# Performance work log

Hardware: AMD Instinct MI355X
Metric: run time of the kernel (lower is better)

Reference implementation:

```python
import jax, jax.numpy as jnp
import numpy as np

DIM = 1024
H = 16
HD = DIM // H
SCALE = HD ** -0.5
LAMBDA_INIT = 0.1
EPS = 1e-6


def setup_inputs() -> dict:
    key0 = jax.random.key(0)
    ks = jax.random.split(key0, 12)
    B, Nq, Nk = 2, 1024, 2048
    w = 0.02
    inp = {
        "query": jax.random.normal(ks[0], (B, Nq, DIM), jnp.float32),
        "key": jax.random.normal(ks[1], (B, Nk, DIM), jnp.float32),
        "value": jax.random.normal(ks[2], (B, Nk, DIM), jnp.float32),
        "qpos": jax.random.randint(ks[3], (B, Nq), 0, Nq, jnp.int32),
        "kpos": jax.random.randint(ks[4], (B, Nk), 0, Nk, jnp.int32),
        "q1_w": jax.random.normal(ks[5], (DIM, DIM), jnp.float32) * w,
        "q2_w": jax.random.normal(ks[6], (DIM, DIM), jnp.float32) * w,
        "kv1_w": jax.random.normal(ks[7], (2 * DIM, DIM), jnp.float32) * w,
        "kv2_w": jax.random.normal(ks[8], (2 * DIM, DIM), jnp.float32) * w,
        "proj_w": jax.random.normal(ks[9], (DIM, DIM), jnp.float32) * w,
        "proj_b": jnp.zeros((DIM,), jnp.float32),
        "norm_w": jnp.ones((DIM,), jnp.float32),
        "lambda_1": jnp.ones((1, H, 1, 1), jnp.float32),
        # layer_idx=0, max_layer=12 -> scale = 1/12
        "lambda_2": jnp.full((1, H, 1, 1), 1.0 - LAMBDA_INIT * (1.0 / 12.0), jnp.float32),
    }
    return inp


def _split_heads(x, B, N):
    # [B, N, DIM] -> [B, H, N, HD]
    return x.reshape(B, N, H, HD).transpose(0, 2, 1, 3)


def reference(query, key, value, qpos, kpos, q1_w, q2_w, kv1_w, kv2_w,
              proj_w, proj_b, norm_w, lambda_1, lambda_2):
    B, Nq, C = query.shape
    Nk = key.shape[1]

    q1 = _split_heads(query @ q1_w.T, B, Nq)
    q2 = _split_heads(query @ q2_w.T, B, Nq)

    kv1 = (key @ kv1_w.T).reshape(B, Nk, 2, H, HD).transpose(2, 0, 3, 1, 4)
    k1, v1 = kv1[0], kv1[1]  # [B, H, Nk, HD]
    kv2 = (key @ kv2_w.T).reshape(B, Nk, 2, H, HD).transpose(2, 0, 3, 1, 4)
    k2 = kv2[0]

    attn1 = jax.nn.softmax(jnp.einsum('bhqd,bhkd->bhqk', q1, k1) * SCALE, axis=-1)
    attn2 = jax.nn.softmax(jnp.einsum('bhqd,bhkd->bhqk', q2, k2) * SCALE, axis=-1)

    lambda_full = lambda_1 - lambda_2 + LAMBDA_INIT  # [1, H, 1, 1]
    diff_attn = attn1 - lambda_full * attn2

    x = jnp.einsum('bhqk,bhkd->bhqd', diff_attn, v1)
    x = x.transpose(0, 2, 1, 3).reshape(B, Nq, C)

    # RMSNorm (computed in float32 like the original)
    xf = x.astype(jnp.float32)
    xf = xf * jax.lax.rsqrt(jnp.mean(xf * xf, axis=-1, keepdims=True) + EPS) * norm_w
    x = xf.astype(x.dtype)

    return x @ proj_w.T + proj_b
```

## Files before the change

kernel.cpp:

```cpp
#include <hip/hip_runtime.h>
#include <cstdint>

typedef unsigned short u16;
typedef __bf16 bf16x8 __attribute__((ext_vector_type(8)));
typedef float f32x4 __attribute__((ext_vector_type(4)));
typedef float f32x16 __attribute__((ext_vector_type(16)));
typedef uint32_t u32x4 __attribute__((ext_vector_type(4)));

#define SCALE_LOG2E (0.125f * 1.44269504088896340736f)

__device__ __forceinline__ u16 f2bf(float f) {
    uint32_t u = __builtin_bit_cast(uint32_t, f);
    u += 0x7fff + ((u >> 16) & 1);
    return (u16)(u >> 16);
}
__device__ __forceinline__ float bf2f(u16 u) {
    return __builtin_bit_cast(float, (uint32_t)u << 16);
}

__device__ __forceinline__ void gload_lds16(const void* g, void* l) {
    __builtin_amdgcn_global_load_lds(
        (__attribute__((address_space(1))) void*)g,
        (__attribute__((address_space(3))) void*)l, 16, 0, 0);
}

__global__ __launch_bounds__(256) void cvt_all(const float* __restrict__ s0,
                                               const float* __restrict__ s1,
                                               const float* __restrict__ s2,
                                               const float* __restrict__ s3,
                                               const float* __restrict__ s4,
                                               const float* __restrict__ s5,
                                               const float* __restrict__ s6,
                                               u16* __restrict__ d0, u16* __restrict__ d1,
                                               u16* __restrict__ d2, u16* __restrict__ d3,
                                               u16* __restrict__ d4) {
    int i = blockIdx.x * 256 + threadIdx.x;
    const float* src;
    u16* dst;
    int off;
    if (i < 524288)       { src = s0; dst = d0; off = i; }
    else if (i < 1572864) { src = s1; dst = d1; off = i - 524288; }
    else if (i < 1835008) { src = s2; dst = d2; off = i - 1572864; }
    else if (i < 2097152) { src = s3; dst = d2 + (size_t)1024 * 1024; off = i - 1835008; }
    else if (i < 2621440) { src = s4; dst = d3; off = i - 2097152; }
    else if (i < 2883584) { src = s5; dst = d3 + (size_t)2048 * 1024; off = i - 2621440; }
    else                  { src = s6; dst = d4; off = i - 2883584; }
    float4 v = ((const float4*)src)[off];
    ushort4 o;
    o.x = f2bf(v.x); o.y = f2bf(v.y); o.z = f2bf(v.z); o.w = f2bf(v.w);
    ((ushort4*)dst)[off] = o;
}

__global__ __launch_bounds__(256) void gemm_qkv(const u16* __restrict__ Xq,
                                                const u16* __restrict__ Wq,
                                                const u16* __restrict__ Xk,
                                                const u16* __restrict__ Wkv,
                                                u16* __restrict__ q1s, u16* __restrict__ q2s,
                                                u16* __restrict__ k1f, u16* __restrict__ v1f,
                                                u16* __restrict__ k2f) {
    __shared__ u16 As[128 * 32];
    __shared__ u16 Bs[128 * 32];
    const int K = 1024;
    const int bid = blockIdx.x;
    int mode, bm, bn;
    const u16 *A, *B;
    if (bid < 256) {
        mode = 0; bm = bid >> 4; bn = bid & 15; A = Xq; B = Wq;
    } else {
        int t = bid - 256;
        mode = 1; bm = t / 24; bn = t % 24; A = Xk; B = Wkv;
    }
    const int tid = threadIdx.x;
    const int l = tid & 63, w = tid >> 6;
    const int c = l & 15, g = l >> 4;
    const int wr = w >> 1, wc = w & 1;

    f32x4 acc[4][4];
#pragma unroll
    for (int i = 0; i < 4; i++)
#pragma unroll
        for (int j = 0; j < 4; j++) acc[i][j] = f32x4{0.f, 0.f, 0.f, 0.f};

    const u16* Abase = A + (size_t)(bm * 128) * K;
    const u16* Bbase = B + (size_t)(bn * 128) * K;
    const int r0 = 32 * w + (l >> 2);
    const int ch = (l & 3) * 8;

    for (int kb = 0; kb < K; kb += 32) {
        gload_lds16(Abase + (size_t)r0 * K + kb + ch,        As + 32 * w * 32);
        gload_lds16(Abase + (size_t)(r0 + 16) * K + kb + ch, As + (32 * w + 16) * 32);
        gload_lds16(Bbase + (size_t)r0 * K + kb + ch,        Bs + 32 * w * 32);
        gload_lds16(Bbase + (size_t)(r0 + 16) * K + kb + ch, Bs + (32 * w + 16) * 32);
        __syncthreads();
        bf16x8 af[4], bfr[4];
#pragma unroll
        for (int mi = 0; mi < 4; mi++)
            af[mi] = *(const bf16x8*)&As[(64 * wr + 16 * mi + c) * 32 + 8 * g];
#pragma unroll
        for (int ni = 0; ni < 4; ni++)
            bfr[ni] = *(const bf16x8*)&Bs[(64 * wc + 16 * ni + c) * 32 + 8 * g];
#pragma unroll
        for (int mi = 0; mi < 4; mi++)
#pragma unroll
            for (int ni = 0; ni < 4; ni++)
                acc[mi][ni] = __builtin_amdgcn_mfma_f32_16x16x32_bf16(
                    af[mi], bfr[ni], acc[mi][ni], 0, 0, 0);
        __syncthreads();
    }

#pragma unroll
    for (int mi = 0; mi < 4; mi++)
#pragma unroll
        for (int ni = 0; ni < 4; ni++)
#pragma unroll
            for (int j = 0; j < 4; j++) {
                int m = bm * 128 + 64 * wr + 16 * mi + 4 * g + j;
                int n = bn * 128 + 64 * wc + 16 * ni + c;
                float v = acc[mi][ni][j];
                if (mode == 0) {
                    int b = m >> 10, nq = m & 1023;
                    int half = n >> 10, nn = n & 1023;
                    int h = nn >> 6, hd = nn & 63;
                    u16* dst = half ? q2s : q1s;
                    dst[(size_t)((b * 16 + h) * 1024 + nq) * 64 + hd] = f2bf(v * SCALE_LOG2E);
                } else {
                    int b = m >> 11, nk = m & 2047;
                    if (n < 1024) {
                        int h = n >> 6, hd = n & 63;
                        int bh = b * 16 + h;
                        size_t idx = ((size_t)(bh * 64 + (nk >> 5)) * 4 + (hd >> 4)) * 512
                                   + (((hd >> 3) & 1) * 32 + (nk & 31)) * 8 + (hd & 7);
                        k1f[idx] = f2bf(v);
                    } else if (n < 2048) {
                        int nn = n - 1024, h = nn >> 6, hd = nn & 63;
                        int bh = b * 16 + h;
                        size_t idx = ((size_t)(bh * 128 + (nk >> 4)) * 2 + (hd >> 5)) * 512
                                   + (((nk >> 3) & 1) * 32 + (hd & 31)) * 8 + (nk & 7);
                        v1f[idx] = f2bf(v);
                    } else {
                        int nn = n - 2048, h = nn >> 6, hd = nn & 63;
                        int bh = b * 16 + h;
                        size_t idx = ((size_t)(bh * 64 + (nk >> 5)) * 4 + (hd >> 4)) * 512
                                   + (((hd >> 3) & 1) * 32 + (nk & 31)) * 8 + (hd & 7);
                        k2f[idx] = f2bf(v);
                    }
                }
            }
}

__global__ __launch_bounds__(256) void gemm_proj(const u16* __restrict__ A,
                                                 const u16* __restrict__ B,
                                                 float* __restrict__ fo,
                                                 const float* __restrict__ bias) {
    __shared__ u16 As[128 * 32];
    __shared__ u16 Bs[64 * 32];
    const int K = 1024;
    const int bm = blockIdx.x >> 4, bn = blockIdx.x & 15;
    const int tid = threadIdx.x;
    const int l = tid & 63, w = tid >> 6;
    const int c = l & 15, g = l >> 4;
    const int wr = w >> 1, wc = w & 1;

    f32x4 acc[4][2];
#pragma unroll
    for (int i = 0; i < 4; i++)
#pragma unroll
        for (int j = 0; j < 2; j++) acc[i][j] = f32x4{0.f, 0.f, 0.f, 0.f};

    const u16* Abase = A + (size_t)(bm * 128) * K;
    const u16* Bbase = B + (size_t)(bn * 64) * K;
    const int rA = 32 * w + (l >> 2);
    const int rB = 16 * w + (l >> 2);
    const int ch = (l & 3) * 8;

    for (int kb = 0; kb < K; kb += 32) {
        gload_lds16(Abase + (size_t)rA * K + kb + ch,        As + 32 * w * 32);
        gload_lds16(Abase + (size_t)(rA + 16) * K + kb + ch, As + (32 * w + 16) * 32);
        gload_lds16(Bbase + (size_t)rB * K + kb + ch,        Bs + 16 * w * 32);
        __syncthreads();
        bf16x8 af[4], bfr[2];
#pragma unroll
        for (int mi = 0; mi < 4; mi++)
            af[mi] = *(const bf16x8*)&As[(64 * wr + 16 * mi + c) * 32 + 8 * g];
#pragma unroll
        for (int ni = 0; ni < 2; ni++)
            bfr[ni] = *(const bf16x8*)&Bs[(32 * wc + 16 * ni + c) * 32 + 8 * g];
#pragma unroll
        for (int mi = 0; mi < 4; mi++)
#pragma unroll
            for (int ni = 0; ni < 2; ni++)
                acc[mi][ni] = __builtin_amdgcn_mfma_f32_16x16x32_bf16(
                    af[mi], bfr[ni], acc[mi][ni], 0, 0, 0);
        __syncthreads();
    }

#pragma unroll
    for (int mi = 0; mi < 4; mi++)
#pragma unroll
        for (int ni = 0; ni < 2; ni++)
#pragma unroll
            for (int j = 0; j < 4; j++) {
                int m = bm * 128 + 64 * wr + 16 * mi + 4 * g + j;
                int n = bn * 64 + 32 * wc + 16 * ni + c;
                fo[(size_t)m * 1024 + n] = acc[mi][ni][j] + bias[n];
            }
}

__global__ __launch_bounds__(256) void attn_kernel(const u16* __restrict__ q1s,
                                                   const u16* __restrict__ q2s,
                                                   const u16* __restrict__ k1fm,
                                                   const u16* __restrict__ k2fm,
                                                   const u16* __restrict__ v1fm,
                                                   u16* __restrict__ Opart,
                                                   float* __restrict__ Lpart) {
    const int tid = threadIdx.x;
    const int l = tid & 63, w = tid >> 6;
    const int c5 = l & 31, hf = l >> 5;
    const int bid = blockIdx.x;
    const int xcd = bid & 7, slot = bid >> 3;
    const int bh = xcd * 4 + (slot >> 5);
    const int r = slot & 31;
    const int qt = r >> 2, s = r & 3;
    const int b = bh >> 4, head = bh & 15;
    const int q0 = qt * 128 + w * 32;

    bf16x8 qB1[4], qB2[4];
    {
        const u16* p1 = q1s + (size_t)(bh * 1024 + q0 + c5) * 64 + 8 * hf;
        const u16* p2 = q2s + (size_t)(bh * 1024 + q0 + c5) * 64 + 8 * hf;
#pragma unroll
        for (int d = 0; d < 4; d++) {
            qB1[d] = *(const bf16x8*)(p1 + 16 * d);
            qB2[d] = *(const bf16x8*)(p2 + 16 * d);
        }
    }

    f32x16 O1[2], O2[2];
#pragma unroll
    for (int dh = 0; dh < 2; dh++)
#pragma unroll
        for (int i = 0; i < 16; i++) { O1[dh][i] = 0.f; O2[dh][i] = 0.f; }
    float la1 = 0.f, la2 = 0.f;

    const u16* k1t = k1fm + (size_t)bh * 64 * 2048;
    const u16* k2t = k2fm + (size_t)bh * 64 * 2048;
    const u16* vt  = v1fm + (size_t)bh * 128 * 1024;

    for (int it = 0; it < 16; it++) {
        const int t32 = s * 16 + it;
        const u16* p1 = k1t + (size_t)t32 * 2048 + l * 8;
        const u16* p2 = k2t + (size_t)t32 * 2048 + l * 8;
        const u16* pv = vt + (size_t)t32 * 2048 + l * 8;

        bf16x8 kA1[4], kA2[4];
#pragma unroll
        for (int d = 0; d < 4; d++) {
            kA1[d] = *(const bf16x8*)(p1 + d * 512);
            kA2[d] = *(const bf16x8*)(p2 + d * 512);
        }
        bf16x8 vB[2][2];
#pragma unroll
        for (int kk = 0; kk < 2; kk++)
#pragma unroll
            for (int dh = 0; dh < 2; dh++)
                vB[dh][kk] = *(const bf16x8*)(pv + (2 * kk + dh) * 512);

        {
            f32x16 S;
#pragma unroll
            for (int i = 0; i < 16; i++) S[i] = 0.f;
#pragma unroll
            for (int d = 0; d < 4; d++)
                S = __builtin_amdgcn_mfma_f32_32x32x16_bf16(kA1[d], qB1[d], S, 0, 0, 0);
            uint32_t dpk[8];
#pragma unroll
            for (int i = 0; i < 8; i++) {
                float pa = __builtin_exp2f(S[2 * i]);
                float pb = __builtin_exp2f(S[2 * i + 1]);
                la1 += pa + pb;
                asm("v_cvt_pk_bf16_f32 %0, %1, %2" : "=v"(dpk[i]) : "v"(pa), "v"(pb));
            }
            uint32_t a0 = dpk[0], b0 = dpk[2], a1 = dpk[1], b1 = dpk[3];
            asm("v_permlane32_swap_b32 %0, %1" : "+v"(a0), "+v"(b0));
            asm("v_permlane32_swap_b32 %0, %1" : "+v"(a1), "+v"(b1));
            u32x4 t0 = {a0, a1, b0, b1};
            bf16x8 pf0 = __builtin_bit_cast(bf16x8, t0);
            uint32_t a2 = dpk[4], b2 = dpk[6], a3 = dpk[5], b3 = dpk[7];
            asm("v_permlane32_swap_b32 %0, %1" : "+v"(a2), "+v"(b2));
            asm("v_permlane32_swap_b32 %0, %1" : "+v"(a3), "+v"(b3));
            u32x4 t1 = {a2, a3, b2, b3};
            bf16x8 pf1 = __builtin_bit_cast(bf16x8, t1);
#pragma unroll
            for (int dh = 0; dh < 2; dh++) {
                O1[dh] = __builtin_amdgcn_mfma_f32_32x32x16_bf16(pf0, vB[dh][0], O1[dh], 0, 0, 0);
                O1[dh] = __builtin_amdgcn_mfma_f32_32x32x16_bf16(pf1, vB[dh][1], O1[dh], 0, 0, 0);
            }
        }
        {
            f32x16 S;
#pragma unroll
            for (int i = 0; i < 16; i++) S[i] = 0.f;
#pragma unroll
            for (int d = 0; d < 4; d++)
                S = __builtin_amdgcn_mfma_f32_32x32x16_bf16(kA2[d], qB2[d], S, 0, 0, 0);
            uint32_t dpk[8];
#pragma unroll
            for (int i = 0; i < 8; i++) {
                float pa = __builtin_exp2f(S[2 * i]);
                float pb = __builtin_exp2f(S[2 * i + 1]);
                la2 += pa + pb;
                asm("v_cvt_pk_bf16_f32 %0, %1, %2" : "=v"(dpk[i]) : "v"(pa), "v"(pb));
            }
            uint32_t a0 = dpk[0], b0 = dpk[2], a1 = dpk[1], b1 = dpk[3];
            asm("v_permlane32_swap_b32 %0, %1" : "+v"(a0), "+v"(b0));
            asm("v_permlane32_swap_b32 %0, %1" : "+v"(a1), "+v"(b1));
            u32x4 t0 = {a0, a1, b0, b1};
            bf16x8 pf0 = __builtin_bit_cast(bf16x8, t0);
            uint32_t a2 = dpk[4], b2 = dpk[6], a3 = dpk[5], b3 = dpk[7];
            asm("v_permlane32_swap_b32 %0, %1" : "+v"(a2), "+v"(b2));
            asm("v_permlane32_swap_b32 %0, %1" : "+v"(a3), "+v"(b3));
            u32x4 t1 = {a2, a3, b2, b3};
            bf16x8 pf1 = __builtin_bit_cast(bf16x8, t1);
#pragma unroll
            for (int dh = 0; dh < 2; dh++) {
                O2[dh] = __builtin_amdgcn_mfma_f32_32x32x16_bf16(pf0, vB[dh][0], O2[dh], 0, 0, 0);
                O2[dh] = __builtin_amdgcn_mfma_f32_32x32x16_bf16(pf1, vB[dh][1], O2[dh], 0, 0, 0);
            }
        }
    }

    la1 += __shfl_xor(la1, 32, 64);
    la2 += __shfl_xor(la2, 32, 64);

#pragma unroll
    for (int dh = 0; dh < 2; dh++)
#pragma unroll
        for (int rr = 0; rr < 16; rr++) {
            int qrow = (rr & 3) + 8 * (rr >> 2) + 4 * hf;
            size_t rowg = (size_t)b * 1024 + q0 + qrow;
            size_t col = head * 64 + dh * 32 + c5;
            Opart[((size_t)(s * 2 + 0) * 2048 + rowg) * 1024 + col] = f2bf(O1[dh][rr]);
            Opart[((size_t)(s * 2 + 1) * 2048 + rowg) * 1024 + col] = f2bf(O2[dh][rr]);
        }
    if (hf == 0) {
        size_t rowg = (size_t)b * 1024 + q0 + c5;
        Lpart[((size_t)(s * 2 + 0) * 2048 + rowg) * 16 + head] = la1;
        Lpart[((size_t)(s * 2 + 1) * 2048 + rowg) * 16 + head] = la2;
    }
}

__global__ __launch_bounds__(256) void combine_rms(const u16* __restrict__ Opart,
                                                   const float* __restrict__ Lpart,
                                                   const float* __restrict__ lam1,
                                                   const float* __restrict__ lam2,
                                                   const float* __restrict__ nw,
                                                   u16* __restrict__ xn) {
    const int row = blockIdx.x, t = threadIdx.x;
    const int h = t >> 4;
    float a1[4] = {0.f, 0.f, 0.f, 0.f}, a2[4] = {0.f, 0.f, 0.f, 0.f};
    float li1 = 0.f, li2 = 0.f;
#pragma unroll
    for (int s = 0; s < 4; s++) {
        ushort4 u1 = ((const ushort4*)(Opart + ((size_t)(s * 2 + 0) * 2048 + row) * 1024))[t];
        ushort4 u2 = ((const ushort4*)(Opart + ((size_t)(s * 2 + 1) * 2048 + row) * 1024))[t];
        a1[0] += bf2f(u1.x); a1[1] += bf2f(u1.y); a1[2] += bf2f(u1.z); a1[3] += bf2f(u1.w);
        a2[0] += bf2f(u2.x); a2[1] += bf2f(u2.y); a2[2] += bf2f(u2.z); a2[3] += bf2f(u2.w);
        li1 += Lpart[((size_t)(s * 2 + 0) * 2048 + row) * 16 + h];
        li2 += Lpart[((size_t)(s * 2 + 1) * 2048 + row) * 16 + h];
    }
    float lam = lam1[h] - lam2[h] + 0.1f;
    float i1 = 1.0f / li1, i2 = lam / li2;
    float x0 = a1[0] * i1 - a2[0] * i2;
    float x1 = a1[1] * i1 - a2[1] * i2;
    float x2 = a1[2] * i1 - a2[2] * i2;
    float x3 = a1[3] * i1 - a2[3] * i2;
    float ss = x0 * x0 + x1 * x1 + x2 * x2 + x3 * x3;
#pragma unroll
    for (int off = 1; off < 64; off <<= 1) ss += __shfl_xor(ss, off, 64);
    __shared__ float ws4[4];
    if ((t & 63) == 0) ws4[t >> 6] = ss;
    __syncthreads();
    float tot = ws4[0] + ws4[1] + ws4[2] + ws4[3];
    float rs = rsqrtf(tot * (1.0f / 1024.0f) + 1e-6f);
    float4 wv = ((const float4*)nw)[t];
    ushort4 o;
    o.x = f2bf(x0 * rs * wv.x);
    o.y = f2bf(x1 * rs * wv.y);
    o.z = f2bf(x2 * rs * wv.z);
    o.w = f2bf(x3 * rs * wv.w);
    ((ushort4*)(xn + (size_t)row * 1024))[t] = o;
}

extern "C" void kernel_launch(void* const* d_in, const int* in_sizes, int n_in,
                              void* d_out, int out_size, void* d_ws, size_t ws_size,
                              hipStream_t stream) {
    const float* query  = (const float*)d_in[0];
    const float* key    = (const float*)d_in[1];
    const float* q1_w   = (const float*)d_in[5];
    const float* q2_w   = (const float*)d_in[6];
    const float* kv1_w  = (const float*)d_in[7];
    const float* kv2_w  = (const float*)d_in[8];
    const float* proj_w = (const float*)d_in[9];
    const float* proj_b = (const float*)d_in[10];
    const float* norm_w = (const float*)d_in[11];
    const float* lam1   = (const float*)d_in[12];
    const float* lam2   = (const float*)d_in[13];
    float* out = (float*)d_out;

    char* ws = (char*)d_ws;
    size_t off = 0;
    auto alloc = [&](size_t bytes) {
        void* p = ws + off;
        off += (bytes + 255) & ~(size_t)255;
        return p;
    };
    u16* Xq   = (u16*)alloc((size_t)2048 * 1024 * 2);
    u16* Xk   = (u16*)alloc((size_t)4096 * 1024 * 2);
    u16* Wq   = (u16*)alloc((size_t)2048 * 1024 * 2);
    u16* Wkv  = (u16*)alloc((size_t)3072 * 1024 * 2);
    u16* Wp   = (u16*)alloc((size_t)1024 * 1024 * 2);
    u16* q1sb = (u16*)alloc((size_t)32 * 1024 * 64 * 2);
    u16* q2sb = (u16*)alloc((size_t)32 * 1024 * 64 * 2);
    u16* k1fb = (u16*)alloc((size_t)32 * 2048 * 64 * 2);
    u16* k2fb = (u16*)alloc((size_t)32 * 2048 * 64 * 2);
    u16* v1fb = (u16*)alloc((size_t)32 * 64 * 2048 * 2);
    u16* Opart = (u16*)alloc((size_t)8 * 2048 * 1024 * 2);
    float* Lpart = (float*)alloc((size_t)8 * 2048 * 16 * 4);
    u16* xn   = (u16*)alloc((size_t)2048 * 1024 * 2);

    cvt_all<<<12288, 256, 0, stream>>>(query, key, q1_w, q2_w, kv1_w, kv2_w, proj_w,
                                       Xq, Xk, Wq, Wkv, Wp);

    gemm_qkv<<<1024, 256, 0, stream>>>(Xq, Wq, Xk, Wkv, q1sb, q2sb, k1fb, v1fb, k2fb);

    attn_kernel<<<1024, 256, 0, stream>>>(q1sb, q2sb, k1fb, k2fb, v1fb, Opart, Lpart);

    combine_rms<<<2048, 256, 0, stream>>>(Opart, Lpart, lam1, lam2, norm_w, xn);

    gemm_proj<<<256, 256, 0, stream>>>(xn, Wp, out, proj_b);
}
```

Measured before the change: 266.7 us.

## Double-buffer GEMM LDS tiles, swizzle LDS, and swap operands for vectorized stores

Both GEMM kernels now double-buffer their LDS tiles, so the next K-slice is prefetched while the current one feeds MFMAs, leaving one barrier per iteration instead of two. LDS columns are XOR-swizzled to cut bank conflicts on fragment reads. The QKV GEMM swaps operands so weights are the M side, which lets the epilogue write four contiguous bf16 values per store. Q is also stored in the same fragment-major layout as K, so the attention kernel's Q loads change to match. Double buffering doubles LDS use per block, which may lower occupancy.

```diff
diff --git a/kernel.cpp b/kernel.cpp
--- a/kernel.cpp
+++ b/kernel.cpp
@@ -51,24 +51,24 @@
     ((ushort4*)dst)[off] = o;
 }
 
-__global__ __launch_bounds__(256) void gemm_qkv(const u16* __restrict__ Xq,
-                                                const u16* __restrict__ Wq,
+__global__ __launch_bounds__(256) void gemm_qkv(const u16* __restrict__ Wq,
+                                                const u16* __restrict__ Xq,
+                                                const u16* __restrict__ Wkv,
                                                 const u16* __restrict__ Xk,
-                                                const u16* __restrict__ Wkv,
                                                 u16* __restrict__ q1s, u16* __restrict__ q2s,
                                                 u16* __restrict__ k1f, u16* __restrict__ v1f,
                                                 u16* __restrict__ k2f) {
-    __shared__ u16 As[128 * 32];
-    __shared__ u16 Bs[128 * 32];
+    __shared__ u16 As[2][128 * 32];
+    __shared__ u16 Bs[2][128 * 32];
     const int K = 1024;
     const int bid = blockIdx.x;
     int mode, bm, bn;
     const u16 *A, *B;
     if (bid < 256) {
-        mode = 0; bm = bid >> 4; bn = bid & 15; A = Xq; B = Wq;
+        mode = 0; bm = bid >> 4; bn = bid & 15; A = Wq; B = Xq;
     } else {
         int t = bid - 256;
-        mode = 1; bm = t / 24; bn = t % 24; A = Xk; B = Wkv;
+        mode = 1; bm = t % 24; bn = t / 24; A = Wkv; B = Xk;
     }
     const int tid = threadIdx.x;
     const int l = tid & 63, w = tid >> 6;
@@ -84,21 +84,32 @@
     const u16* Abase = A + (size_t)(bm * 128) * K;
     const u16* Bbase = B + (size_t)(bn * 128) * K;
     const int r0 = 32 * w + (l >> 2);
-    const int ch = (l & 3) * 8;
-
-    for (int kb = 0; kb < K; kb += 32) {
-        gload_lds16(Abase + (size_t)r0 * K + kb + ch,        As + 32 * w * 32);
-        gload_lds16(Abase + (size_t)(r0 + 16) * K + kb + ch, As + (32 * w + 16) * 32);
-        gload_lds16(Bbase + (size_t)r0 * K + kb + ch,        Bs + 32 * w * 32);
-        gload_lds16(Bbase + (size_t)(r0 + 16) * K + kb + ch, Bs + (32 * w + 16) * 32);
-        __syncthreads();
+    const int chsw = ((l & 3) ^ ((l >> 3) & 3)) * 8;
+
+    const int gsw = 8 * (g ^ ((c >> 1) & 3));
+
+    int cur = 0;
+    gload_lds16(Abase + (size_t)r0 * K + chsw,        &As[0][32 * w * 32]);
+    gload_lds16(Abase + (size_t)(r0 + 16) * K + chsw, &As[0][(32 * w + 16) * 32]);
+    gload_lds16(Bbase + (size_t)r0 * K + chsw,        &Bs[0][32 * w * 32]);
+    gload_lds16(Bbase + (size_t)(r0 + 16) * K + chsw, &Bs[0][(32 * w + 16) * 32]);
+    __syncthreads();
+
+    for (int t = 0; t < 32; ++t) {
+        if (t < 31) {
+            const int kb = (t + 1) * 32;
+            gload_lds16(Abase + (size_t)r0 * K + kb + chsw,        &As[cur ^ 1][32 * w * 32]);
+            gload_lds16(Abase + (size_t)(r0 + 16) * K + kb + chsw, &As[cur ^ 1][(32 * w + 16) * 32]);
+            gload_lds16(Bbase + (size_t)r0 * K + kb + chsw,        &Bs[cur ^ 1][32 * w * 32]);
+            gload_lds16(Bbase + (size_t)(r0 + 16) * K + kb + chsw, &Bs[cur ^ 1][(32 * w + 16) * 32]);
+        }
         bf16x8 af[4], bfr[4];
 #pragma unroll
         for (int mi = 0; mi < 4; mi++)
-            af[mi] = *(const bf16x8*)&As[(64 * wr + 16 * mi + c) * 32 + 8 * g];
+            af[mi] = *(const bf16x8*)&As[cur][(64 * wr + 16 * mi + c) * 32 + gsw];
 #pragma unroll
         for (int ni = 0; ni < 4; ni++)
-            bfr[ni] = *(const bf16x8*)&Bs[(64 * wc + 16 * ni + c) * 32 + 8 * g];
+            bfr[ni] = *(const bf16x8*)&Bs[cur][(64 * wc + 16 * ni + c) * 32 + gsw];
 #pragma unroll
         for (int mi = 0; mi < 4; mi++)
 #pragma unroll
@@ -106,54 +117,65 @@
                 acc[mi][ni] = __builtin_amdgcn_mfma_f32_16x16x32_bf16(
                     af[mi], bfr[ni], acc[mi][ni], 0, 0, 0);
         __syncthreads();
-    }
-
-#pragma unroll
-    for (int mi = 0; mi < 4; mi++)
-#pragma unroll
-        for (int ni = 0; ni < 4; ni++)
-#pragma unroll
-            for (int j = 0; j < 4; j++) {
-                int m = bm * 128 + 64 * wr + 16 * mi + 4 * g + j;
-                int n = bn * 128 + 64 * wc + 16 * ni + c;
-                float v = acc[mi][ni][j];
-                if (mode == 0) {
-                    int b = m >> 10, nq = m & 1023;
-                    int half = n >> 10, nn = n & 1023;
-                    int h = nn >> 6, hd = nn & 63;
-                    u16* dst = half ? q2s : q1s;
-                    dst[(size_t)((b * 16 + h) * 1024 + nq) * 64 + hd] = f2bf(v * SCALE_LOG2E);
-                } else {
-                    int b = m >> 11, nk = m & 2047;
-                    if (n < 1024) {
-                        int h = n >> 6, hd = n & 63;
-                        int bh = b * 16 + h;
-                        size_t idx = ((size_t)(bh * 64 + (nk >> 5)) * 4 + (hd >> 4)) * 512
-                                   + (((hd >> 3) & 1) * 32 + (nk & 31)) * 8 + (hd & 7);
-                        k1f[idx] = f2bf(v);
-                    } else if (n < 2048) {
-                        int nn = n - 1024, h = nn >> 6, hd = nn & 63;
-                        int bh = b * 16 + h;
+        cur ^= 1;
+    }
+
+#pragma unroll
+    for (int mi = 0; mi < 4; mi++) {
+        const int m0 = bm * 128 + 64 * wr + 16 * mi + 4 * g;
+#pragma unroll
+        for (int ni = 0; ni < 4; ni++) {
+            const int n = bn * 128 + 64 * wc + 16 * ni + c;
+            f32x4 v = acc[mi][ni];
+            if (mode == 0) {
+                int half = m0 >> 10, feat = m0 & 1023;
+                int h = feat >> 6, hd0 = feat & 63;
+                int b = n >> 10, nq = n & 1023;
+                int bh = b * 16 + h;
+                u16* dst = half ? q2s : q1s;
+                size_t idx = ((size_t)(bh * 32 + (nq >> 5)) * 4 + (hd0 >> 4)) * 512
+                           + (((hd0 >> 3) & 1) * 32 + (nq & 31)) * 8 + (hd0 & 7);
+                ushort4 o;
+                o.x = f2bf(v[0] * SCALE_LOG2E); o.y = f2bf(v[1] * SCALE_LOG2E);
+                o.z = f2bf(v[2] * SCALE_LOG2E); o.w = f2bf(v[3] * SCALE_LOG2E);
+                *(ushort4*)(dst + idx) = o;
+            } else {
+                int b = n >> 11, nk = n & 2047;
+                if (m0 < 1024) {
+                    int h = m0 >> 6, hd0 = m0 & 63, bh = b * 16 + h;
+                    size_t idx = ((size_t)(bh * 64 + (nk >> 5)) * 4 + (hd0 >> 4)) * 512
+                               + (((hd0 >> 3) & 1) * 32 + (nk & 31)) * 8 + (hd0 & 7);
+                    ushort4 o;
+                    o.x = f2bf(v[0]); o.y = f2bf(v[1]); o.z = f2bf(v[2]); o.w = f2bf(v[3]);
+                    *(ushort4*)(k1f + idx) = o;
+                } else if (m0 < 2048) {
+                    int feat = m0 - 1024, h = feat >> 6, hd0 = feat & 63, bh = b * 16 + h;
+#pragma unroll
+                    for (int j = 0; j < 4; j++) {
+                        int hd = hd0 + j;
                         size_t idx = ((size_t)(bh * 128 + (nk >> 4)) * 2 + (hd >> 5)) * 512
                                    + (((nk >> 3) & 1) * 32 + (hd & 31)) * 8 + (nk & 7);
-                        v1f[idx] = f2bf(v);
-                    } else {
-                        int nn = n - 2048, h = nn >> 6, hd = nn & 63;
-                        int bh = b * 16 + h;
-                        size_t idx = ((size_t)(bh * 64 + (nk >> 5)) * 4 + (hd >> 4)) * 512
-                                   + (((hd >> 3) & 1) * 32 + (nk & 31)) * 8 + (hd & 7);
-                        k2f[idx] = f2bf(v);
+                        v1f[idx] = f2bf(v[j]);
                     }
+                } else {
+                    int feat = m0 - 2048, h = feat >> 6, hd0 = feat & 63, bh = b * 16 + h;
+                    size_t idx = ((size_t)(bh * 64 + (nk >> 5)) * 4 + (hd0 >> 4)) * 512
+                               + (((hd0 >> 3) & 1) * 32 + (nk & 31)) * 8 + (hd0 & 7);
+                    ushort4 o;
+                    o.x = f2bf(v[0]); o.y = f2bf(v[1]); o.z = f2bf(v[2]); o.w = f2bf(v[3]);
+                    *(ushort4*)(k2f + idx) = o;
                 }
             }
+        }
+    }
 }
 
 __global__ __launch_bounds__(256) void gemm_proj(const u16* __restrict__ A,
                                                  const u16* __restrict__ B,
                                                  float* __restrict__ fo,
                                                  const float* __restrict__ bias) {
-    __shared__ u16 As[128 * 32];
-    __shared__ u16 Bs[64 * 32];
+    __shared__ u16 As[2][128 * 32];
+    __shared__ u16 Bs[2][64 * 32];
     const int K = 1024;
     const int bm = blockIdx.x >> 4, bn = blockIdx.x & 15;
     const int tid = threadIdx.x;
@@ -171,20 +193,29 @@
     const u16* Bbase = B + (size_t)(bn * 64) * K;
     const int rA = 32 * w + (l >> 2);
     const int rB = 16 * w + (l >> 2);
-    const int ch = (l & 3) * 8;
-
-    for (int kb = 0; kb < K; kb += 32) {
-        gload_lds16(Abase + (size_t)rA * K + kb + ch,        As + 32 * w * 32);
-        gload_lds16(Abase + (size_t)(rA + 16) * K + kb + ch, As + (32 * w + 16) * 32);
-        gload_lds16(Bbase + (size_t)rB * K + kb + ch,        Bs + 16 * w * 32);
-        __syncthreads();
+    const int chsw = ((l & 3) ^ ((l >> 3) & 3)) * 8;
+    const int gsw = 8 * (g ^ ((c >> 1) & 3));
+
+    int cur = 0;
+    gload_lds16(Abase + (size_t)rA * K + chsw,        &As[0][32 * w * 32]);
+    gload_lds16(Abase + (size_t)(rA + 16) * K + chsw, &As[0][(32 * w + 16) * 32]);
+    gload_lds16(Bbase + (size_t)rB * K + chsw,        &Bs[0][16 * w * 32]);
+    __syncthreads();
+
+    for (int t = 0; t < 32; ++t) {
+        if (t < 31) {
+            const int kb = (t + 1) * 32;
+            gload_lds16(Abase + (size_t)rA * K + kb + chsw,        &As[cur ^ 1][32 * w * 32]);
+            gload_lds16(Abase + (size_t)(rA + 16) * K + kb + chsw, &As[cur ^ 1][(32 * w + 16) * 32]);
+            gload_lds16(Bbase + (size_t)rB * K + kb + chsw,        &Bs[cur ^ 1][16 * w * 32]);
+        }
         bf16x8 af[4], bfr[2];
 #pragma unroll
         for (int mi = 0; mi < 4; mi++)
-            af[mi] = *(const bf16x8*)&As[(64 * wr + 16 * mi + c) * 32 + 8 * g];
+            af[mi] = *(const bf16x8*)&As[cur][(64 * wr + 16 * mi + c) * 32 + gsw];
 #pragma unroll
         for (int ni = 0; ni < 2; ni++)
-            bfr[ni] = *(const bf16x8*)&Bs[(32 * wc + 16 * ni + c) * 32 + 8 * g];
+            bfr[ni] = *(const bf16x8*)&Bs[cur][(32 * wc + 16 * ni + c) * 32 + gsw];
 #pragma unroll
         for (int mi = 0; mi < 4; mi++)
 #pragma unroll
@@ -192,6 +223,7 @@
                 acc[mi][ni] = __builtin_amdgcn_mfma_f32_16x16x32_bf16(
                     af[mi], bfr[ni], acc[mi][ni], 0, 0, 0);
         __syncthreads();
+        cur ^= 1;
     }
 
 #pragma unroll
@@ -226,12 +258,12 @@
 
     bf16x8 qB1[4], qB2[4];
     {
-        const u16* p1 = q1s + (size_t)(bh * 1024 + q0 + c5) * 64 + 8 * hf;
-        const u16* p2 = q2s + (size_t)(bh * 1024 + q0 + c5) * 64 + 8 * hf;
+        const u16* p1 = q1s + ((size_t)(bh * 32 + (q0 >> 5)) * 4) * 512 + l * 8;
+        const u16* p2 = q2s + ((size_t)(bh * 32 + (q0 >> 5)) * 4) * 512 + l * 8;
 #pragma unroll
         for (int d = 0; d < 4; d++) {
-            qB1[d] = *(const bf16x8*)(p1 + 16 * d);
-            qB2[d] = *(const bf16x8*)(p2 + 16 * d);
+            qB1[d] = *(const bf16x8*)(p1 + d * 512);
+            qB2[d] = *(const bf16x8*)(p2 + d * 512);
         }
     }
 
@@ -431,7 +463,7 @@
     cvt_all<<<12288, 256, 0, stream>>>(query, key, q1_w, q2_w, kv1_w, kv2_w, proj_w,
                                        Xq, Xk, Wq, Wkv, Wp);
 
-    gemm_qkv<<<1024, 256, 0, stream>>>(Xq, Wq, Xk, Wkv, q1sb, q2sb, k1fb, v1fb, k2fb);
+    gemm_qkv<<<1024, 256, 0, stream>>>(Wq, Xq, Wkv, Xk, q1sb, q2sb, k1fb, v1fb, k2fb);
 
     attn_kernel<<<1024, 256, 0, stream>>>(q1sb, q2sb, k1fb, k2fb, v1fb, Opart, Lpart);
 
```

Result: faster. 260.4 us (-2.4%).
